# Optimization experiments

Hardware: AMD Instinct MI355X
Metric: run time of the kernel (lower is better)

## Reference

```python
import jax, jax.numpy as jnp
import numpy as np

DIM, H, MAX_K, RADIUS, KNN_K, ALPHA, LN_EPS = 128, 4, 32, 0.3, 8, 2, 1e-5
DH = DIM // H
SCALE = DH ** -0.5


def _layernorm(x, w, b):
    mu = jnp.mean(x, axis=-1, keepdims=True)
    var = jnp.mean((x - mu) ** 2, axis=-1, keepdims=True)
    return (x - mu) * jax.lax.rsqrt(var + LN_EPS) * w + b


def setup_inputs() -> dict:
    key = jax.random.key(0)
    ks = jax.random.split(key, 12)
    N, M = 50000, 2500
    init = lambda k, shape: (jax.random.normal(k, shape, jnp.float32) * 0.02)
    return {
        "xyz": jax.random.normal(ks[0], (N, 3), jnp.float32),
        "feats": jax.random.normal(ks[1], (N, DIM), jnp.float32),
        "Wq": init(ks[2], (DIM, DIM)),
        "Wk": init(ks[3], (DIM, DIM)),
        "Wv": init(ks[4], (DIM, DIM)),
        "Wo": init(ks[5], (DIM, DIM)),
        "bo": jnp.zeros((DIM,), jnp.float32),
        "n1w": jnp.ones((DIM,), jnp.float32),
        "n1b": jnp.zeros((DIM,), jnp.float32),
        "n2w": jnp.ones((DIM,), jnp.float32),
        "n2b": jnp.zeros((DIM,), jnp.float32),
        "W1": init(ks[6], (DIM, 4 * DIM)),
        "b1": jnp.zeros((4 * DIM,), jnp.float32),
        "W2": init(ks[7], (4 * DIM, DIM)),
        "b2": jnp.zeros((DIM,), jnp.float32),
        "Wp": init(ks[8], (DIM, DIM)),
        "bp": jnp.zeros((DIM,), jnp.float32),
        "idx_center": jax.random.randint(ks[9], (M,), 0, N),
    }


def reference(xyz, feats, Wq, Wk, Wv, Wo, bo, n1w, n1b, n2w, n2b, W1, b1, W2, b2, Wp, bp, idx_center):
    M = idx_center.shape[0]
    center_xyz = xyz[idx_center]          # (M,3)
    center_feat = feats[idx_center]       # (M,C)

    # euclidean distance matrix (M,N) via |a|^2+|b|^2-2ab, safe sqrt (0-grad at 0 like torch.cdist)
    d2 = (jnp.sum(center_xyz ** 2, -1)[:, None] + jnp.sum(xyz ** 2, -1)[None, :]
          - 2.0 * center_xyz @ xyz.T)
    d2 = jnp.maximum(d2, 0.0)
    pos = d2 > 0
    dist = jnp.where(pos, jnp.sqrt(jnp.where(pos, d2, 1.0)), 0.0)  # (M,N)

    # ball query: mask + top-max_k smallest distances
    nbr_mask = dist < RADIUS
    nbr_mask = nbr_mask.at[jnp.arange(M), idx_center].set(True)
    dist_masked = jnp.where(nbr_mask, dist, jnp.inf)
    neg_d, nbr_idx = jax.lax.top_k(-dist_masked, MAX_K)   # (M,K)
    nbr_dist = -neg_d
    mask_valid = jnp.isfinite(nbr_dist)                    # (M,K)

    # gather neighbor feats, zero where invalid
    nbr_feats = jnp.where(mask_valid[..., None], feats[nbr_idx], 0.0)  # (M,K,C)

    # masked local attention per center (tiny heads)
    q = (center_feat @ Wq).reshape(M, H, DH)                       # (M,H,D)
    k = (nbr_feats @ Wk).reshape(M, MAX_K, H, DH).transpose(0, 2, 1, 3)  # (M,H,K,D)
    v = (nbr_feats @ Wv).reshape(M, MAX_K, H, DH).transpose(0, 2, 1, 3)
    attn = jnp.einsum('mhd,mhkd->mhk', q * SCALE, k)
    attn = jnp.where(mask_valid[:, None, :], attn, -1e9)
    attn = jax.nn.softmax(attn, axis=-1)
    out = jnp.einsum('mhk,mhkd->mhd', attn, v)
    # faithful to torch: transpose(1,2) before flatten -> (M, D, H) layout
    out = jnp.swapaxes(out, 1, 2).reshape(M, DIM)
    upd = out @ Wo + bo

    cf = center_feat + _layernorm(upd, n1w, n1b)
    ffn = jax.nn.relu(cf @ W1 + b1) @ W2 + b2
    cf = cf + _layernorm(ffn, n2w, n2b)

    # KNN inverse-distance-weighted upsample back to all N points
    neg_v, knn_idx = jax.lax.top_k(-dist.T, KNN_K)   # (N,k)
    knn_dist = -neg_v
    w = 1.0 / (knn_dist + 1e-6) ** ALPHA
    w = w / jnp.sum(w, axis=-1, keepdims=True)
    out_feats = jnp.einsum('nk,nkc->nc', w, cf[knn_idx])  # (N,C)
    out_feats = out_feats + jax.nn.relu(out_feats @ Wp + bp)
    return feats + out_feats
```

## Files before the change

### kernel.cpp

```cpp
#include <hip/hip_runtime.h>
#include <hip/hip_bf16.h>
#include <stdint.h>

#define DIM    128
#define KMAX   32
#define LN_EPS 1e-5f
#define ATT_SCALE 0.17677669529663687f
#define CAND   2048
#define WTOT   214400
#define PB     32
#define NSTR   36
#define KSTR   132

typedef unsigned long long u64;
static __device__ __forceinline__ float bf2f(__hip_bfloat16 x) { return __bfloat162float(x); }

static __device__ __forceinline__ float norm32(float x, float y, float z) {
    return __fadd_rn(__fadd_rn(__fmul_rn(x, x), __fmul_rn(y, y)), __fmul_rn(z, z));
}
static __device__ __forceinline__ float d2_32(float cx, float cy, float cz, float cw,
                                              float px, float py, float pz, float pw) {
    float dot = __fmaf_rn(cz, pz, __fmaf_rn(cy, py, __fmul_rn(cx, px)));
    return __fsub_rn(__fadd_rn(cw, pw), __fmul_rn(2.0f, dot));
}
static __device__ __forceinline__ float d2_to_dist(float d2) {
    d2 = fmaxf(d2, 0.0f);
    return (d2 > 0.0f) ? __fsqrt_rn(d2) : 0.0f;
}
static __device__ __forceinline__ float dist32(float cx, float cy, float cz, float cw,
                                               float px, float py, float pz, float pw) {
    return d2_to_dist(d2_32(cx, cy, cz, cw, px, py, pz, pw));
}

static __device__ __forceinline__ float ldf(const void* p, int f32, size_t i) {
    return f32 ? ((const float*)p)[i] : bf2f(((const __hip_bfloat16*)p)[i]);
}
static __device__ __forceinline__ int ldidx(const void* p, int i64, int m) {
    return i64 ? ((const int*)p)[2 * m] : ((const int*)p)[m];
}

struct Ptrs { const void* p[18]; int sz[18]; };

__global__ void probe_dtypes(Ptrs P, int* __restrict__ fl) {
    int j = threadIdx.x;
    if (j >= 18) return;
    const void* x = P.p[j];
    int sz = P.sz[j];
    int flag = 0;
    if (j == 17) {
        const int* ip = (const int*)x;
        int odd_zero = 1, even_nz = 0;
        for (int k = 0; k < 8 && 2 * k + 1 < sz * 2; ++k) {
            if (ip[2 * k + 1] != 0) odd_zero = 0;
            if (ip[2 * k] != 0) even_nz = 1;
        }
        flag = (odd_zero && even_nz) ? 1 : 0;
    } else {
        const __hip_bfloat16* hp = (const __hip_bfloat16*)x;
        int n = sz < 256 ? sz : 256;
        for (int i = 0; i < n; ++i) {
            float w = bf2f(hp[i]);
            if (w != w || fabsf(w) > 1000.0f) { flag = 1; break; }
        }
        if ((j == 7 || j == 9) && bf2f(hp[0]) == 0.0f) flag = 1;
    }
    fl[j] = flag;
}

__global__ __launch_bounds__(256) void conv_params(Ptrs P, const int* __restrict__ fl,
                                                   float* __restrict__ Wf) {
    int i = blockIdx.x * 256 + threadIdx.x;
    if (i >= WTOT) return;
    int j, off;
    if      (i < 16384)  { j = 2;  off = i; }
    else if (i < 32768)  { j = 3;  off = i - 16384; }
    else if (i < 49152)  { j = 4;  off = i - 32768; }
    else if (i < 65536)  { j = 5;  off = i - 49152; }
    else if (i < 131072) { j = 11; off = i - 65536; }
    else if (i < 196608) { j = 13; off = i - 131072; }
    else if (i < 212992) { j = 15; off = i - 196608; }
    else if (i < 213120) { j = 6;  off = i - 212992; }
    else if (i < 213248) { j = 7;  off = i - 213120; }
    else if (i < 213376) { j = 8;  off = i - 213248; }
    else if (i < 213504) { j = 9;  off = i - 213376; }
    else if (i < 213632) { j = 10; off = i - 213504; }
    else if (i < 214144) { j = 12; off = i - 213632; }
    else if (i < 214272) { j = 14; off = i - 214144; }
    else                 { j = 16; off = i - 214272; }
    Wf[i] = ldf(P.p[j], fl[j], off);
}

__global__ void prep_pts(const void* __restrict__ xyz, const int* __restrict__ fl,
                         float4* __restrict__ pnt4, int N) {
    int i = blockIdx.x * 256 + threadIdx.x;
    if (i < N) {
        int f = fl[0];
        float x = ldf(xyz, f, 3 * i + 0), y = ldf(xyz, f, 3 * i + 1), z = ldf(xyz, f, 3 * i + 2);
        pnt4[i] = make_float4(x, y, z, norm32(x, y, z));
    }
}

__global__ void prep_ctrs(const void* __restrict__ idxc, const int* __restrict__ fl,
                          const float4* __restrict__ pnt4, float4* __restrict__ cent4,
                          int M, int N) {
    int m = blockIdx.x * 256 + threadIdx.x;
    if (m < M) {
        int c = ldidx(idxc, fl[17], m);
        c = (c >= 0 && c < N) ? c : 0;
        cent4[m] = pnt4[c];
    }
}

__global__ __launch_bounds__(256) void ball_scan(
    const float4* __restrict__ pnt4,
    const float4* __restrict__ cent4,
    int N, int* __restrict__ nbr_g) {

    __shared__ u64 key[CAND];
    __shared__ int s_cnt, s_ni[KMAX];

    int m = blockIdx.x, tid = threadIdx.x;
    float4 cc4 = cent4[m];

    if (tid == 0) s_cnt = 0;
    if (tid < KMAX) s_ni[tid] = -1;
    __syncthreads();

    for (int i = tid; i < N; i += 256) {
        float4 p = pnt4[i];
        float d2 = d2_32(cc4.x, cc4.y, cc4.z, cc4.w, p.x, p.y, p.z, p.w);
        if (d2 < 0.0901f) {
            float dist = d2_to_dist(d2);
            if (dist < 0.3f) {
                int pos = atomicAdd(&s_cnt, 1);
                if (pos < CAND)
                    key[pos] = ((u64)__float_as_uint(dist) << 32) | (unsigned)i;
            }
        }
    }
    __syncthreads();
    int cnt = min(s_cnt, CAND);

    for (int i = tid; i < cnt; i += 256) {
        u64 ki = key[i];
        int r = 0;
        for (int j = 0; j < cnt; ++j) r += (key[j] < ki) ? 1 : 0;
        if (r < KMAX) s_ni[r] = (int)(unsigned)(ki & 0xFFFFFFFFULL);
    }
    __syncthreads();
    if (tid < KMAX) nbr_g[m * KMAX + tid] = s_ni[tid];
}

#define NFT(cc, kk) R[(cc) * NSTR + (kk)]
#define SKV(kk, col) R[(kk) * KSTR + (col)]

__global__ __launch_bounds__(256) void attn_ffn(
    const int* __restrict__ nbr_g,
    const void* __restrict__ feats,
    const void* __restrict__ idxc,
    const int* __restrict__ fl,
    const float* __restrict__ Wf,
    float* __restrict__ cf_out, int N) {

    const float* Wqf = Wf;
    const float* Wkf = Wf + 16384;
    const float* Wvf = Wf + 32768;
    const float* Wof = Wf + 49152;
    const float* W1f = Wf + 65536;
    const float* W2f = Wf + 131072;
    const float* Pf  = Wf + 212992;

    __shared__ __align__(16) float R[128 * NSTR];
    __shared__ int   s_ni[KMAX];
    __shared__ __align__(16) float s_cf[DIM], s_q[DIM], s_attn[DIM], s_ao[DIM], s_x[DIM];
    __shared__ float s_red[4];

    int m = blockIdx.x, tid = threadIdx.x;
    int lane = tid & 63, wv = tid >> 6;
    int f1 = fl[1];
    int c = ldidx(idxc, fl[17], m);
    c = (c >= 0 && c < N) ? c : 0;

    if (tid < KMAX) s_ni[tid] = nbr_g[m * KMAX + tid];
    if (tid < 128) s_cf[tid] = ldf(feats, f1, (size_t)c * DIM + tid);
    __syncthreads();
    for (int t = tid; t < KMAX * DIM; t += 256) {
        int kk = t >> 7, cc = t & 127;
        int idx = s_ni[kk];
        float v = (idx >= 0 && idx < N) ? ldf(feats, f1, (size_t)idx * DIM + cc) : 0.0f;
        NFT(cc, kk) = v;
    }
    __syncthreads();

    if (tid < 128) {
        float acc = 0.0f;
#pragma unroll 4
        for (int i = 0; i < DIM; i += 4) {
            float4 a = *(const float4*)&s_cf[i];
            acc = fmaf(a.x, Wqf[(i + 0) * DIM + tid], acc);
            acc = fmaf(a.y, Wqf[(i + 1) * DIM + tid], acc);
            acc = fmaf(a.z, Wqf[(i + 2) * DIM + tid], acc);
            acc = fmaf(a.w, Wqf[(i + 3) * DIM + tid], acc);
        }
        s_q[tid] = acc;
    }

    int kq = tid >> 5, cq = tid & 31;
    int k0 = kq * 4, c0 = cq * 4;
    float ka[4][4], va[4][4];
#pragma unroll
    for (int j = 0; j < 4; ++j)
#pragma unroll
        for (int cc2 = 0; cc2 < 4; ++cc2) { ka[j][cc2] = 0.0f; va[j][cc2] = 0.0f; }

#pragma unroll 2
    for (int i = 0; i < DIM; ++i) {
        float4 n  = *(const float4*)&NFT(i, k0);
        float4 wk = *(const float4*)&Wkf[i * DIM + c0];
        float4 wv4 = *(const float4*)&Wvf[i * DIM + c0];
#pragma unroll
        for (int j = 0; j < 4; ++j) {
            float nj = (&n.x)[j];
            ka[j][0] = fmaf(nj, wk.x, ka[j][0]);
            ka[j][1] = fmaf(nj, wk.y, ka[j][1]);
            ka[j][2] = fmaf(nj, wk.z, ka[j][2]);
            ka[j][3] = fmaf(nj, wk.w, ka[j][3]);
            va[j][0] = fmaf(nj, wv4.x, va[j][0]);
            va[j][1] = fmaf(nj, wv4.y, va[j][1]);
            va[j][2] = fmaf(nj, wv4.z, va[j][2]);
            va[j][3] = fmaf(nj, wv4.w, va[j][3]);
        }
    }
    __syncthreads();
#pragma unroll
    for (int j = 0; j < 4; ++j)
        *(float4*)&SKV(k0 + j, c0) = make_float4(ka[j][0], ka[j][1], ka[j][2], ka[j][3]);
    __syncthreads();

    if (tid < 128) {
        int h = tid >> 5, kk = tid & 31;
        float s = 0.0f;
#pragma unroll
        for (int d = 0; d < 32; ++d)
            s = fmaf(s_q[h * 32 + d], SKV(kk, h * 32 + d), s);
        s *= ATT_SCALE;
        if (s_ni[kk] < 0) s = -1e9f;
        float mx = s;
        for (int off = 16; off; off >>= 1) mx = fmaxf(mx, __shfl_xor(mx, off, 32));
        float e = expf(s - mx);
        float sm = e;
        for (int off = 16; off; off >>= 1) sm += __shfl_xor(sm, off, 32);
        sm = (sm > 0.0f) ? sm : 1.0f;
        s_attn[tid] = e / sm;
    }
    __syncthreads();
#pragma unroll
    for (int j = 0; j < 4; ++j)
        *(float4*)&SKV(k0 + j, c0) = make_float4(va[j][0], va[j][1], va[j][2], va[j][3]);
    __syncthreads();

    if (tid < 128) {
        int h = tid >> 5, d = tid & 31;
        float o = 0.0f;
#pragma unroll
        for (int kk = 0; kk < KMAX; ++kk)
            o = fmaf(s_attn[h * 32 + kk], SKV(kk, h * 32 + d), o);
        s_ao[d * 4 + h] = o;
    }
    __syncthreads();

    float upd = 0.0f;
    if (tid < 128) {
        upd = Pf[0 + tid];
#pragma unroll 4
        for (int i = 0; i < DIM; i += 4) {
            float4 a = *(const float4*)&s_ao[i];
            upd = fmaf(a.x, Wof[(i + 0) * DIM + tid], upd);
            upd = fmaf(a.y, Wof[(i + 1) * DIM + tid], upd);
            upd = fmaf(a.z, Wof[(i + 2) * DIM + tid], upd);
            upd = fmaf(a.w, Wof[(i + 3) * DIM + tid], upd);
        }
        float sum = upd;
        for (int off = 32; off; off >>= 1) sum += __shfl_xor(sum, off, 64);
        if (lane == 0) s_red[wv] = sum;
    }
    __syncthreads();
    float mu = (s_red[0] + s_red[1]) * (1.0f / 128.0f);
    float xc = upd - mu;
    if (tid < 128) {
        float q2 = xc * xc;
        for (int off = 32; off; off >>= 1) q2 += __shfl_xor(q2, off, 64);
        if (lane == 0) s_red[2 + wv] = q2;
    }
    __syncthreads();
    float var = (s_red[2] + s_red[3]) * (1.0f / 128.0f);
    float cf1 = 0.0f;
    if (tid < 128) {
        float rs = 1.0f / sqrtf(var + LN_EPS);
        float ln1 = fmaf(xc * rs, Pf[128 + tid], Pf[256 + tid]);
        cf1 = s_cf[tid] + ln1;
        s_x[tid] = cf1;
    }
    __syncthreads();

    float* s_h = R;
    float* s_part = R + 512;
#pragma unroll
    for (int jj = 0; jj < 2; ++jj) {
        int j = jj * 256 + tid;
        float a = Pf[640 + j];
#pragma unroll 4
        for (int i = 0; i < DIM; i += 4) {
            float4 v = *(const float4*)&s_x[i];
            a = fmaf(v.x, W1f[(i + 0) * 512 + j], a);
            a = fmaf(v.y, W1f[(i + 1) * 512 + j], a);
            a = fmaf(v.z, W1f[(i + 2) * 512 + j], a);
            a = fmaf(v.w, W1f[(i + 3) * 512 + j], a);
        }
        s_h[j] = fmaxf(a, 0.0f);
    }
    __syncthreads();

    int col = tid & 127;
    int half = tid >> 7;
    float f2 = (half == 0) ? Pf[1152 + col] : 0.0f;
    {
        int i0 = half * 256;
#pragma unroll 4
        for (int i = i0; i < i0 + 256; i += 4) {
            float4 v = *(const float4*)&s_h[i];
            f2 = fmaf(v.x, W2f[(i + 0) * DIM + col], f2);
            f2 = fmaf(v.y, W2f[(i + 1) * DIM + col], f2);
            f2 = fmaf(v.z, W2f[(i + 2) * DIM + col], f2);
            f2 = fmaf(v.w, W2f[(i + 3) * DIM + col], f2);
        }
    }
    float* s_part2 = s_part;
    s_part2[tid] = f2;
    __syncthreads();
    float ffn = 0.0f;
    if (tid < 128) {
        ffn = s_part2[tid] + s_part2[tid + 128];
        float sum = ffn;
        for (int off = 32; off; off >>= 1) sum += __shfl_xor(sum, off, 64);
        if (lane == 0) s_red[wv] = sum;
    }
    __syncthreads();
    mu = (s_red[0] + s_red[1]) * (1.0f / 128.0f);
    xc = ffn - mu;
    if (tid < 128) {
        float q2 = xc * xc;
        for (int off = 32; off; off >>= 1) q2 += __shfl_xor(q2, off, 64);
        if (lane == 0) s_red[2 + wv] = q2;
    }
    __syncthreads();
    var = (s_red[2] + s_red[3]) * (1.0f / 128.0f);
    if (tid < 128) {
        float rs2 = 1.0f / sqrtf(var + LN_EPS);
        float ln2 = fmaf(xc * rs2, Pf[384 + tid], Pf[512 + tid]);
        cf_out[(size_t)m * DIM + tid] = cf1 + ln2;
    }
}

#define CSWAP(a, b) { if ((b) < (a)) { u64 t_ = (a); (a) = (b); (b) = t_; } }

__global__ __launch_bounds__(256) void knn_select(
    const float4* __restrict__ pnt4,
    const float4* __restrict__ cent4,
    const float* __restrict__ cf,
    float* __restrict__ upg,
    int N, int M) {

    __shared__ u64 s_buf[4][64];
    __shared__ u64 s_srt[4][8];
    __shared__ int s_cnt[4];

    int lane = threadIdx.x & 63;
    int wv   = threadIdx.x >> 6;
    int p = blockIdx.x * 4 + wv;
    bool own = (p < N);

    float4 pp = make_float4(0.f, 0.f, 0.f, 0.f);
    if (own) pp = pnt4[p];

    if (lane == 0) s_cnt[wv] = 0;
    __syncthreads();

    float vmn = 3.4e38f;
    for (int j = lane; j < M; j += 64) {
        float4 cc = cent4[j];
        float d2 = d2_32(cc.x, cc.y, cc.z, cc.w, pp.x, pp.y, pp.z, pp.w);
        vmn = fminf(vmn, d2);
    }
    float vv = vmn, T = 0.0f;
#pragma unroll
    for (int e = 0; e < 8; ++e) {
        float mv = vv;
        for (int off = 32; off; off >>= 1) mv = fminf(mv, __shfl_xor(mv, off, 64));
        T = mv;
        if (vv == mv) vv = 3.4e38f;
    }
    float Tuse = fmaxf(T, 0.0f) * 1.0000019073486328f;

    for (int j = lane; j < M; j += 64) {
        float4 cc = cent4[j];
        float d2 = d2_32(cc.x, cc.y, cc.z, cc.w, pp.x, pp.y, pp.z, pp.w);
        if (d2 <= Tuse) {
            float dist = d2_to_dist(d2);
            u64 key = ((u64)__float_as_uint(dist) << 32) | (unsigned)j;
            int pos = atomicAdd(&s_cnt[wv], 1);
            if (pos < 64) s_buf[wv][pos] = key;
        }
    }
    __syncthreads();
    int cnt = s_cnt[wv];

    int   ki[8];
    float w8[8];
    float wsum = 0.0f;

    if (cnt <= 64 && M >= 8) {
        u64 myk = (lane < cnt) ? s_buf[wv][lane] : ~0ULL;
        int r = 0;
        for (int i = 0; i < cnt; ++i) {
            u64 o = s_buf[wv][i];
            r += (o < myk) ? 1 : 0;
        }
        if (lane < cnt && r < 8) s_srt[wv][r] = myk;
#pragma unroll
        for (int e = 0; e < 8; ++e) {
            u64 gm = s_srt[wv][e];
            float d = __uint_as_float((unsigned)(gm >> 32));
            int ci = (int)(unsigned)(gm & 0xFFFFFFFFULL);
            ci = (ci >= 0 && ci < M) ? ci : 0;
            float t = __fadd_rn(d, 1e-6f);
            float w = 1.0f / __fmul_rn(t, t);
            wsum += w;
            ki[e] = ci;
            w8[e] = w;
        }
    } else {
        u64 f0 = ~0ULL, f1_ = ~0ULL, f2_ = ~0ULL, f3 = ~0ULL,
            f4 = ~0ULL, f5 = ~0ULL, f6 = ~0ULL, f7 = ~0ULL;
        for (int j = lane; j < M; j += 64) {
            float4 cc = cent4[j];
            float dist = dist32(cc.x, cc.y, cc.z, cc.w, pp.x, pp.y, pp.z, pp.w);
            u64 key = ((u64)__float_as_uint(dist) << 32) | (unsigned)j;
            if (key < f7) {
                f7 = key;
                CSWAP(f6, f7); CSWAP(f5, f6); CSWAP(f4, f5); CSWAP(f3, f4);
                CSWAP(f2_, f3); CSWAP(f1_, f2_); CSWAP(f0, f1_);
            }
        }
        int ptr2 = 0;
        u64 cur2 = f0;
        wsum = 0.0f;
#pragma unroll
        for (int e = 0; e < 8; ++e) {
            u64 v = cur2;
            for (int off = 32; off; off >>= 1) {
                u64 o = __shfl_down(v, off, 64);
                v = (o < v) ? o : v;
            }
            u64 gm = __shfl(v, 0, 64);
            float d = __uint_as_float((unsigned)(gm >> 32));
            int ci = (int)(unsigned)(gm & 0xFFFFFFFFULL);
            ci = (ci >= 0 && ci < M) ? ci : 0;
            float t = __fadd_rn(d, 1e-6f);
            float w = 1.0f / __fmul_rn(t, t);
            wsum += w;
            ki[e] = ci;
            w8[e] = w;
            if (cur2 == gm) {
                ptr2++;
                cur2 = (ptr2 == 1) ? f1_ : (ptr2 == 2) ? f2_ : (ptr2 == 3) ? f3 :
                       (ptr2 == 4) ? f4 : (ptr2 == 5) ? f5 : (ptr2 == 6) ? f6 :
                       (ptr2 == 7) ? f7 : ~0ULL;
            }
        }
    }

    float inv = 1.0f / wsum;
#pragma unroll
    for (int e = 0; e < 8; ++e) w8[e] *= inv;

    int c0 = lane, c1 = lane + 64;
    float up0 = 0.0f, up1 = 0.0f;
#pragma unroll
    for (int k = 0; k < 8; ++k) {
        const float* row = cf + (size_t)ki[k] * DIM;
        up0 = fmaf(w8[k], row[c0], up0);
        up1 = fmaf(w8[k], row[c1], up1);
    }

    if (own) {
        upg[(size_t)p * DIM + c0] = up0;
        upg[(size_t)p * DIM + c1] = up1;
    }
}

__global__ __launch_bounds__(256) void wp_out(
    const float* __restrict__ Wf,
    const void* __restrict__ feats,
    const int* __restrict__ fl,
    float* __restrict__ out,
    int N) {

    const float* Wpf = Wf + 196608;
    const float* bpf = Wf + 212992 + 1280;

    __shared__ __align__(16) float s_up[PB][132];

    int tid = threadIdx.x;
    int p0 = blockIdx.x * PB;

    for (int f = tid; f < PB * 32; f += 256) {
        int p = f >> 5, i4 = (f & 31) << 2;
        float4 v = make_float4(0.f, 0.f, 0.f, 0.f);
        if (p0 + p < N) v = *(const float4*)&out[(size_t)(p0 + p) * DIM + i4];
        *(float4*)&s_up[p][i4] = v;
    }
    __syncthreads();

    int cq = tid & 31, pq = tid >> 5;
    int c0 = cq << 2;
    int pA = pq << 2;

    float a00 = 0.f, a01 = 0.f, a02 = 0.f, a03 = 0.f;
    float a10 = 0.f, a11 = 0.f, a12 = 0.f, a13 = 0.f;
    float a20 = 0.f, a21 = 0.f, a22 = 0.f, a23 = 0.f;
    float a30 = 0.f, a31 = 0.f, a32 = 0.f, a33 = 0.f;

#pragma unroll 4
    for (int i = 0; i < DIM; ++i) {
        float4 w = *(const float4*)&Wpf[(size_t)i * DIM + c0];
        float u0 = s_up[pA + 0][i];
        float u1 = s_up[pA + 1][i];
        float u2 = s_up[pA + 2][i];
        float u3 = s_up[pA + 3][i];
        a00 = fmaf(u0, w.x, a00); a01 = fmaf(u0, w.y, a01);
        a02 = fmaf(u0, w.z, a02); a03 = fmaf(u0, w.w, a03);
        a10 = fmaf(u1, w.x, a10); a11 = fmaf(u1, w.y, a11);
        a12 = fmaf(u1, w.z, a12); a13 = fmaf(u1, w.w, a13);
        a20 = fmaf(u2, w.x, a20); a21 = fmaf(u2, w.y, a21);
        a22 = fmaf(u2, w.z, a22); a23 = fmaf(u2, w.w, a23);
        a30 = fmaf(u3, w.x, a30); a31 = fmaf(u3, w.y, a31);
        a32 = fmaf(u3, w.z, a32); a33 = fmaf(u3, w.w, a33);
    }

    int f1v = fl[1];
    float4 bp4 = make_float4(bpf[c0 + 0], bpf[c0 + 1], bpf[c0 + 2], bpf[c0 + 3]);

    float accs[4][4] = {{a00, a01, a02, a03}, {a10, a11, a12, a13},
                        {a20, a21, a22, a23}, {a30, a31, a32, a33}};
#pragma unroll
    for (int a = 0; a < 4; ++a) {
        int p = p0 + pA + a;
        if (p < N) {
            float4 u = *(const float4*)&s_up[pA + a][c0];
            float4 o;
            o.x = ldf(feats, f1v, (size_t)p * DIM + c0 + 0) + u.x + fmaxf(bp4.x + accs[a][0], 0.0f);
            o.y = ldf(feats, f1v, (size_t)p * DIM + c0 + 1) + u.y + fmaxf(bp4.y + accs[a][1], 0.0f);
            o.z = ldf(feats, f1v, (size_t)p * DIM + c0 + 2) + u.z + fmaxf(bp4.z + accs[a][2], 0.0f);
            o.w = ldf(feats, f1v, (size_t)p * DIM + c0 + 3) + u.w + fmaxf(bp4.w + accs[a][3], 0.0f);
            *(float4*)&out[(size_t)p * DIM + c0] = o;
        }
    }
}

extern "C" void kernel_launch(void* const* d_in, const int* in_sizes, int n_in,
                              void* d_out, int out_size, void* d_ws, size_t ws_size,
                              hipStream_t stream) {
    int N = in_sizes[0] / 3;
    int M = in_sizes[17];

    Ptrs P;
    for (int j = 0; j < 18; ++j) { P.p[j] = d_in[j]; P.sz[j] = in_sizes[j]; }

    size_t off = 0;
    auto alloc = [&](size_t bytes) -> void* {
        off = (off + 255) & ~(size_t)255;
        void* p = (void*)((char*)d_ws + off);
        off += bytes;
        return p;
    };
    int*    fl    = (int*)alloc(32 * 4);
    float*  Wf    = (float*)alloc((size_t)WTOT * 4);
    float4* pnt4  = (float4*)alloc((size_t)N * 16);
    float4* cent4 = (float4*)alloc((size_t)M * 16);
    float*  cfbuf = (float*)alloc((size_t)M * DIM * 4);
    int*    nbr   = (int*)alloc((size_t)M * KMAX * 4);

    probe_dtypes<<<1, 32, 0, stream>>>(P, fl);
    conv_params<<<(WTOT + 255) / 256, 256, 0, stream>>>(P, fl, Wf);
    prep_pts<<<(N + 255) / 256, 256, 0, stream>>>(d_in[0], fl, pnt4, N);
    prep_ctrs<<<(M + 255) / 256, 256, 0, stream>>>(d_in[17], fl, pnt4, cent4, M, N);
    ball_scan<<<M, 256, 0, stream>>>(pnt4, cent4, N, nbr);
    attn_ffn<<<M, 256, 0, stream>>>(nbr, d_in[1], d_in[17], fl, Wf, cfbuf, N);
    knn_select<<<(N + 3) / 4, 256, 0, stream>>>(pnt4, cent4, cfbuf, (float*)d_out, N, M);
    wp_out<<<(N + PB - 1) / PB, 256, 0, stream>>>(Wf, d_in[1], fl, (float*)d_out, N);
}
```

Before: 563.8 us.

## Process two centers per block in attn_ffn to use all 256 threads

attn_ffn now handles two centers per block, so all 256 threads do useful work in the q projection, attention, Wo, LayerNorm and FFN stages, where half the threads used to sit idle. Each weight-matrix row read from global memory now serves two centers, and the grid is halved. The K/V projection tile grows to 8 rows per thread, which raises register pressure. The kernel also gets a launch_bounds occupancy hint of 4 and a larger LDS footprint.

```diff
diff --git a/kernel.cpp b/kernel.cpp
--- a/kernel.cpp
+++ b/kernel.cpp
@@ -9,7 +9,7 @@
 #define CAND   2048
 #define WTOT   214400
 #define PB     32
-#define NSTR   36
+#define NSTR2  72
 #define KSTR   132
 
 typedef unsigned long long u64;
@@ -151,16 +151,16 @@
     if (tid < KMAX) nbr_g[m * KMAX + tid] = s_ni[tid];
 }
 
-#define NFT(cc, kk) R[(cc) * NSTR + (kk)]
-#define SKV(kk, col) R[(kk) * KSTR + (col)]
-
-__global__ __launch_bounds__(256) void attn_ffn(
+#define NFT2(cc, kk) R[(cc) * NSTR2 + (kk)]
+#define SKV2(kk, col) R[(kk) * KSTR + (col)]
+
+__global__ __launch_bounds__(256, 4) void attn_ffn(
     const int* __restrict__ nbr_g,
     const void* __restrict__ feats,
     const void* __restrict__ idxc,
     const int* __restrict__ fl,
     const float* __restrict__ Wf,
-    float* __restrict__ cf_out, int N) {
+    float* __restrict__ cf_out, int N, int M) {
 
     const float* Wqf = Wf;
     const float* Wkf = Wf + 16384;
@@ -170,57 +170,54 @@
     const float* W2f = Wf + 131072;
     const float* Pf  = Wf + 212992;
 
-    __shared__ __align__(16) float R[128 * NSTR];
-    __shared__ int   s_ni[KMAX];
-    __shared__ __align__(16) float s_cf[DIM], s_q[DIM], s_attn[DIM], s_ao[DIM], s_x[DIM];
-    __shared__ float s_red[4];
-
-    int m = blockIdx.x, tid = threadIdx.x;
+    __shared__ __align__(16) float R[128 * NSTR2];
+    __shared__ int   s_ni[2 * KMAX];
+    __shared__ __align__(16) float s_cf[256], s_x[256];
+    __shared__ float s_red[8];
+
+    int tid = threadIdx.x;
     int lane = tid & 63, wv = tid >> 6;
-    int f1 = fl[1];
-    int c = ldidx(idxc, fl[17], m);
-    c = (c >= 0 && c < N) ? c : 0;
-
-    if (tid < KMAX) s_ni[tid] = nbr_g[m * KMAX + tid];
-    if (tid < 128) s_cf[tid] = ldf(feats, f1, (size_t)c * DIM + tid);
-    __syncthreads();
-    for (int t = tid; t < KMAX * DIM; t += 256) {
-        int kk = t >> 7, cc = t & 127;
-        int idx = s_ni[kk];
+    int center = tid >> 7, col = tid & 127;
+    int m0 = blockIdx.x * 2;
+    int f1 = fl[1], fi = fl[17];
+
+    if (tid < 64) {
+        int m2 = m0 + (tid >> 5);
+        s_ni[tid] = (m2 < M) ? nbr_g[m2 * KMAX + (tid & 31)] : -1;
+    }
+    {
+        int m2 = m0 + center; m2 = (m2 < M) ? m2 : (M - 1);
+        int c = ldidx(idxc, fi, m2);
+        c = (c >= 0 && c < N) ? c : 0;
+        s_cf[tid] = ldf(feats, f1, (size_t)c * DIM + col);
+    }
+    __syncthreads();
+    for (int t = tid; t < 64 * DIM; t += 256) {
+        int kk2 = t >> 7, cc = t & 127;
+        int idx = s_ni[kk2];
         float v = (idx >= 0 && idx < N) ? ldf(feats, f1, (size_t)idx * DIM + cc) : 0.0f;
-        NFT(cc, kk) = v;
-    }
-    __syncthreads();
-
-    if (tid < 128) {
-        float acc = 0.0f;
-#pragma unroll 4
-        for (int i = 0; i < DIM; i += 4) {
-            float4 a = *(const float4*)&s_cf[i];
-            acc = fmaf(a.x, Wqf[(i + 0) * DIM + tid], acc);
-            acc = fmaf(a.y, Wqf[(i + 1) * DIM + tid], acc);
-            acc = fmaf(a.z, Wqf[(i + 2) * DIM + tid], acc);
-            acc = fmaf(a.w, Wqf[(i + 3) * DIM + tid], acc);
-        }
-        s_q[tid] = acc;
-    }
+        NFT2(cc, kk2) = v;
+    }
+    __syncthreads();
 
     int kq = tid >> 5, cq = tid & 31;
-    int k0 = kq * 4, c0 = cq * 4;
-    float ka[4][4], va[4][4];
-#pragma unroll
-    for (int j = 0; j < 4; ++j)
+    int k0 = kq * 8, c0 = cq * 4;
+    float ka[8][4], va[8][4];
+#pragma unroll
+    for (int j = 0; j < 8; ++j)
 #pragma unroll
         for (int cc2 = 0; cc2 < 4; ++cc2) { ka[j][cc2] = 0.0f; va[j][cc2] = 0.0f; }
 
 #pragma unroll 2
     for (int i = 0; i < DIM; ++i) {
-        float4 n  = *(const float4*)&NFT(i, k0);
-        float4 wk = *(const float4*)&Wkf[i * DIM + c0];
+        float4 n0  = *(const float4*)&NFT2(i, k0);
+        float4 n1  = *(const float4*)&NFT2(i, k0 + 4);
+        float4 wk  = *(const float4*)&Wkf[i * DIM + c0];
         float4 wv4 = *(const float4*)&Wvf[i * DIM + c0];
-#pragma unroll
-        for (int j = 0; j < 4; ++j) {
-            float nj = (&n.x)[j];
+        float nn[8] = {n0.x, n0.y, n0.z, n0.w, n1.x, n1.y, n1.z, n1.w};
+#pragma unroll
+        for (int j = 0; j < 8; ++j) {
+            float nj = nn[j];
             ka[j][0] = fmaf(nj, wk.x, ka[j][0]);
             ka[j][1] = fmaf(nj, wk.y, ka[j][1]);
             ka[j][2] = fmaf(nj, wk.z, ka[j][2]);
@@ -232,19 +229,37 @@
         }
     }
     __syncthreads();
-#pragma unroll
-    for (int j = 0; j < 4; ++j)
-        *(float4*)&SKV(k0 + j, c0) = make_float4(ka[j][0], ka[j][1], ka[j][2], ka[j][3]);
-    __syncthreads();
-
-    if (tid < 128) {
-        int h = tid >> 5, kk = tid & 31;
+
+    float* s_q    = R + 8448;
+    float* s_attn = R + 8704;
+    float* s_ao   = R + 8960;
+
+#pragma unroll
+    for (int j = 0; j < 8; ++j)
+        *(float4*)&SKV2(k0 + j, c0) = make_float4(ka[j][0], ka[j][1], ka[j][2], ka[j][3]);
+    {
+        float acc = 0.0f;
+        const float* cfc = s_cf + center * 128;
+#pragma unroll 4
+        for (int i = 0; i < DIM; i += 4) {
+            float4 a = *(const float4*)&cfc[i];
+            acc = fmaf(a.x, Wqf[(i + 0) * DIM + col], acc);
+            acc = fmaf(a.y, Wqf[(i + 1) * DIM + col], acc);
+            acc = fmaf(a.z, Wqf[(i + 2) * DIM + col], acc);
+            acc = fmaf(a.w, Wqf[(i + 3) * DIM + col], acc);
+        }
+        s_q[tid] = acc;
+    }
+    __syncthreads();
+
+    {
+        int h = (tid >> 5) & 3, kk = tid & 31;
         float s = 0.0f;
 #pragma unroll
         for (int d = 0; d < 32; ++d)
-            s = fmaf(s_q[h * 32 + d], SKV(kk, h * 32 + d), s);
+            s = fmaf(s_q[center * 128 + h * 32 + d], SKV2(center * 32 + kk, h * 32 + d), s);
         s *= ATT_SCALE;
-        if (s_ni[kk] < 0) s = -1e9f;
+        if (s_ni[center * 32 + kk] < 0) s = -1e9f;
         float mx = s;
         for (int off = 16; off; off >>= 1) mx = fmaxf(mx, __shfl_xor(mx, off, 32));
         float e = expf(s - mx);
@@ -255,110 +270,115 @@
     }
     __syncthreads();
 #pragma unroll
-    for (int j = 0; j < 4; ++j)
-        *(float4*)&SKV(k0 + j, c0) = make_float4(va[j][0], va[j][1], va[j][2], va[j][3]);
-    __syncthreads();
-
-    if (tid < 128) {
-        int h = tid >> 5, d = tid & 31;
+    for (int j = 0; j < 8; ++j)
+        *(float4*)&SKV2(k0 + j, c0) = make_float4(va[j][0], va[j][1], va[j][2], va[j][3]);
+    __syncthreads();
+
+    {
+        int h = (tid >> 5) & 3, d = tid & 31;
         float o = 0.0f;
 #pragma unroll
         for (int kk = 0; kk < KMAX; ++kk)
-            o = fmaf(s_attn[h * 32 + kk], SKV(kk, h * 32 + d), o);
-        s_ao[d * 4 + h] = o;
-    }
-    __syncthreads();
-
-    float upd = 0.0f;
-    if (tid < 128) {
-        upd = Pf[0 + tid];
+            o = fmaf(s_attn[center * 128 + h * 32 + kk], SKV2(center * 32 + kk, h * 32 + d), o);
+        s_ao[center * 128 + d * 4 + h] = o;
+    }
+    __syncthreads();
+
+    float upd = Pf[0 + col];
+    {
 #pragma unroll 4
         for (int i = 0; i < DIM; i += 4) {
-            float4 a = *(const float4*)&s_ao[i];
-            upd = fmaf(a.x, Wof[(i + 0) * DIM + tid], upd);
-            upd = fmaf(a.y, Wof[(i + 1) * DIM + tid], upd);
-            upd = fmaf(a.z, Wof[(i + 2) * DIM + tid], upd);
-            upd = fmaf(a.w, Wof[(i + 3) * DIM + tid], upd);
+            float4 a = *(const float4*)&s_ao[center * 128 + i];
+            upd = fmaf(a.x, Wof[(i + 0) * DIM + col], upd);
+            upd = fmaf(a.y, Wof[(i + 1) * DIM + col], upd);
+            upd = fmaf(a.z, Wof[(i + 2) * DIM + col], upd);
+            upd = fmaf(a.w, Wof[(i + 3) * DIM + col], upd);
         }
         float sum = upd;
         for (int off = 32; off; off >>= 1) sum += __shfl_xor(sum, off, 64);
         if (lane == 0) s_red[wv] = sum;
     }
     __syncthreads();
-    float mu = (s_red[0] + s_red[1]) * (1.0f / 128.0f);
+    float mu = (s_red[center * 2] + s_red[center * 2 + 1]) * (1.0f / 128.0f);
     float xc = upd - mu;
-    if (tid < 128) {
+    {
         float q2 = xc * xc;
         for (int off = 32; off; off >>= 1) q2 += __shfl_xor(q2, off, 64);
-        if (lane == 0) s_red[2 + wv] = q2;
-    }
-    __syncthreads();
-    float var = (s_red[2] + s_red[3]) * (1.0f / 128.0f);
-    float cf1 = 0.0f;
-    if (tid < 128) {
+        if (lane == 0) s_red[4 + wv] = q2;
+    }
+    __syncthreads();
+    float var = (s_red[4 + center * 2] + s_red[5 + center * 2]) * (1.0f / 128.0f);
+    float cf1;
+    {
         float rs = 1.0f / sqrtf(var + LN_EPS);
-        float ln1 = fmaf(xc * rs, Pf[128 + tid], Pf[256 + tid]);
+        float ln1 = fmaf(xc * rs, Pf[128 + col], Pf[256 + col]);
         cf1 = s_cf[tid] + ln1;
         s_x[tid] = cf1;
     }
     __syncthreads();
 
     float* s_h = R;
-    float* s_part = R + 512;
-#pragma unroll
-    for (int jj = 0; jj < 2; ++jj) {
-        int j = jj * 256 + tid;
+#pragma unroll
+    for (int jj = 0; jj < 4; ++jj) {
+        int j = col + 128 * jj;
         float a = Pf[640 + j];
 #pragma unroll 4
         for (int i = 0; i < DIM; i += 4) {
-            float4 v = *(const float4*)&s_x[i];
+            float4 v = *(const float4*)&s_x[center * 128 + i];
             a = fmaf(v.x, W1f[(i + 0) * 512 + j], a);
             a = fmaf(v.y, W1f[(i + 1) * 512 + j], a);
             a = fmaf(v.z, W1f[(i + 2) * 512 + j], a);
             a = fmaf(v.w, W1f[(i + 3) * 512 + j], a);
         }
-        s_h[j] = fmaxf(a, 0.0f);
-    }
-    __syncthreads();
-
-    int col = tid & 127;
-    int half = tid >> 7;
-    float f2 = (half == 0) ? Pf[1152 + col] : 0.0f;
-    {
-        int i0 = half * 256;
+        s_h[center * 512 + j] = fmaxf(a, 0.0f);
+    }
+    __syncthreads();
+
+    float fa = Pf[1152 + col];
+    {
+        const float* hc = s_h + center * 512;
 #pragma unroll 4
-        for (int i = i0; i < i0 + 256; i += 4) {
-            float4 v = *(const float4*)&s_h[i];
-            f2 = fmaf(v.x, W2f[(i + 0) * DIM + col], f2);
-            f2 = fmaf(v.y, W2f[(i + 1) * DIM + col], f2);
-            f2 = fmaf(v.z, W2f[(i + 2) * DIM + col], f2);
-            f2 = fmaf(v.w, W2f[(i + 3) * DIM + col], f2);
-        }
-    }
-    float* s_part2 = s_part;
-    s_part2[tid] = f2;
-    __syncthreads();
-    float ffn = 0.0f;
-    if (tid < 128) {
-        ffn = s_part2[tid] + s_part2[tid + 128];
+        for (int i = 0; i < 256; i += 4) {
+            float4 v = *(const float4*)&hc[i];
+            fa = fmaf(v.x, W2f[(i + 0) * DIM + col], fa);
+            fa = fmaf(v.y, W2f[(i + 1) * DIM + col], fa);
+            fa = fmaf(v.z, W2f[(i + 2) * DIM + col], fa);
+            fa = fmaf(v.w, W2f[(i + 3) * DIM + col], fa);
+        }
+    }
+    float fb = 0.0f;
+    {
+        const float* hc = s_h + center * 512;
+#pragma unroll 4
+        for (int i = 256; i < 512; i += 4) {
+            float4 v = *(const float4*)&hc[i];
+            fb = fmaf(v.x, W2f[(i + 0) * DIM + col], fb);
+            fb = fmaf(v.y, W2f[(i + 1) * DIM + col], fb);
+            fb = fmaf(v.z, W2f[(i + 2) * DIM + col], fb);
+            fb = fmaf(v.w, W2f[(i + 3) * DIM + col], fb);
+        }
+    }
+    float ffn = fa + fb;
+    {
         float sum = ffn;
         for (int off = 32; off; off >>= 1) sum += __shfl_xor(sum, off, 64);
         if (lane == 0) s_red[wv] = sum;
     }
     __syncthreads();
-    mu = (s_red[0] + s_red[1]) * (1.0f / 128.0f);
+    mu = (s_red[center * 2] + s_red[center * 2 + 1]) * (1.0f / 128.0f);
     xc = ffn - mu;
-    if (tid < 128) {
+    {
         float q2 = xc * xc;
         for (int off = 32; off; off >>= 1) q2 += __shfl_xor(q2, off, 64);
-        if (lane == 0) s_red[2 + wv] = q2;
-    }
-    __syncthreads();
-    var = (s_red[2] + s_red[3]) * (1.0f / 128.0f);
-    if (tid < 128) {
+        if (lane == 0) s_red[4 + wv] = q2;
+    }
+    __syncthreads();
+    var = (s_red[4 + center * 2] + s_red[5 + center * 2]) * (1.0f / 128.0f);
+    {
         float rs2 = 1.0f / sqrtf(var + LN_EPS);
-        float ln2 = fmaf(xc * rs2, Pf[384 + tid], Pf[512 + tid]);
-        cf_out[(size_t)m * DIM + tid] = cf1 + ln2;
+        float ln2 = fmaf(xc * rs2, Pf[384 + col], Pf[512 + col]);
+        int m2 = m0 + center;
+        if (m2 < M) cf_out[(size_t)m2 * DIM + col] = cf1 + ln2;
     }
 }
 
@@ -596,7 +616,7 @@
     prep_pts<<<(N + 255) / 256, 256, 0, stream>>>(d_in[0], fl, pnt4, N);
     prep_ctrs<<<(M + 255) / 256, 256, 0, stream>>>(d_in[17], fl, pnt4, cent4, M, N);
     ball_scan<<<M, 256, 0, stream>>>(pnt4, cent4, N, nbr);
-    attn_ffn<<<M, 256, 0, stream>>>(nbr, d_in[1], d_in[17], fl, Wf, cfbuf, N);
+    attn_ffn<<<(M + 1) / 2, 256, 0, stream>>>(nbr, d_in[1], d_in[17], fl, Wf, cfbuf, N, M);
     knn_select<<<(N + 3) / 4, 256, 0, stream>>>(pnt4, cent4, cfbuf, (float*)d_out, N, M);
     wp_out<<<(N + PB - 1) / PB, 256, 0, stream>>>(Wf, d_in[1], fl, (float*)d_out, N);
 }
```

New measurement: 553.8 us. Within noise of the previous version (-1.8%).
